# Performance work log

Measured on AMD Instinct MI355X. Metric: run time of the kernel, lower is better.

## Reference

```python
import jax, jax.numpy as jnp
import numpy as np

B, A, I, D = 4, 32, 512, 256


def setup_inputs() -> dict:
    key = jax.random.key(0)
    k0, k1, kw1, kw2, ka1, ka2 = jax.random.split(key, 6)
    return {
        "i0": jax.random.normal(k0, (B, A, I, D), dtype=jnp.float32),
        "i1": jax.random.normal(k1, (B, A, I, D), dtype=jnp.float32),
        "W1": jax.random.normal(kw1, (D, D), dtype=jnp.float32) * 0.02,
        "W2": jax.random.normal(kw2, (D, D), dtype=jnp.float32) * 0.02,
        "attn1": jax.random.normal(ka1, (D, D), dtype=jnp.float32) * 0.02,
        "attn2": jax.random.normal(ka2, (D, D), dtype=jnp.float32) * 0.02,
    }


def reference(i0, i1, W1, W2, attn1, attn2):
    # Bilinear gating scores: sum_j sum_k x1[...,j] * A[j,k] * x0[...,k] -> [b,a,i]
    g0 = jax.nn.sigmoid(jnp.einsum('baij,jk,baik->bai', i1, attn1, i0))
    g1 = jax.nn.sigmoid(jnp.einsum('baij,jk,baik->bai', i0, attn2, i1))
    # Gated residual: x += x * gate
    r0 = i0 + i0 * g0[..., None]
    r1 = i1 + i1 * g1[..., None]
    # Dual projection sum
    return jnp.einsum('baij,jk->baik', r0, W1) + jnp.einsum('baij,jk->baik', r1, W2)
```

## Files before the change

### kernel.cpp

```cpp
#include <hip/hip_runtime.h>

#define D256 256
#define TOTROWS 65536
#define BM 32
#define LDW 264
#define NBLK (TOTROWS / BM)
#define NT 512

typedef unsigned short u16;
typedef unsigned int u32;
typedef __attribute__((ext_vector_type(8))) short bf16x8;
typedef __attribute__((ext_vector_type(16))) float f32x16;

__device__ __forceinline__ float b2f(u16 u) {
  union { u32 i; float f; } v; v.i = ((u32)u) << 16; return v.f;
}
__device__ __forceinline__ u16 f2b(float f) {
  union { float f; u32 i; } v; v.f = f;
  return (u16)((v.i + 0x7fffu + ((v.i >> 16) & 1u)) >> 16);
}
__device__ __forceinline__ u32 f2b2(float lo, float hi) {
  u32 r;
  asm("v_cvt_pk_bf16_f32 %0, %1, %2" : "=v"(r) : "v"(lo), "v"(hi));
  return r;
}

__global__ void build_wfrag(const float* __restrict__ a1,
                            const float* __restrict__ a2,
                            const float* __restrict__ W1,
                            const float* __restrict__ W2,
                            u16* __restrict__ Wf) {
  const int m = blockIdx.y;
  const int idx = blockIdx.x * 256 + threadIdx.x;
  int col, c;
  const float* src;
  if (m < 2) { col = idx >> 5; c = idx & 31; src = m ? a2 : a1; }
  else       { col = idx & 255; c = idx >> 8; src = (m == 3) ? W2 : W1; }
  const int kk0 = c * 8;
  const int p = col >> 5, l31 = col & 31, lhh = c & 1, k = c >> 1;
  const int ln = lhh * 32 + l31;
  u16* dst = Wf + m * 65536 + ((p * 16 + k) * 64 + ln) * 8;
  u16 v[8];
  if (m < 2) {
#pragma unroll
    for (int j = 0; j < 8; j++) v[j] = f2b(src[col * 256 + kk0 + j]);
  } else {
#pragma unroll
    for (int j = 0; j < 8; j++) v[j] = f2b(src[(kk0 + j) * 256 + col]);
  }
  ushort4 lo, hi;
  lo.x = v[0]; lo.y = v[1]; lo.z = v[2]; lo.w = v[3];
  hi.x = v[4]; hi.y = v[5]; hi.z = v[6]; hi.w = v[7];
  ((ushort4*)dst)[0] = lo;
  ((ushort4*)dst)[1] = hi;
}

__device__ __forceinline__ void reduce_accum(float v[16], float* sp,
                                             int l31, int lh) {
#pragma unroll
  for (int r = 0; r < 8; r++) {
    float a = v[r]     + __shfl_xor(v[r],     1, 32);
    float b = v[r + 8] + __shfl_xor(v[r + 8], 1, 32);
    v[r] = (l31 & 1) ? b : a;
  }
#pragma unroll
  for (int r = 0; r < 4; r++) {
    float a = v[r]     + __shfl_xor(v[r],     2, 32);
    float b = v[r + 4] + __shfl_xor(v[r + 4], 2, 32);
    v[r] = (l31 & 2) ? b : a;
  }
#pragma unroll
  for (int r = 0; r < 2; r++) {
    float a = v[r]     + __shfl_xor(v[r],     4, 32);
    float b = v[r + 2] + __shfl_xor(v[r + 2], 4, 32);
    v[r] = (l31 & 4) ? b : a;
  }
  {
    float a = v[0] + __shfl_xor(v[0], 8, 32);
    float b = v[1] + __shfl_xor(v[1], 8, 32);
    v[0] = (l31 & 8) ? b : a;
  }
  v[0] += __shfl_xor(v[0], 16, 32);
  if (l31 < 16) {
    const int i = ((l31 & 1) << 3) | ((l31 & 2) << 1) | ((l31 & 4) >> 1) |
                  ((l31 & 8) >> 3);
    const int row = (i & 3) + 8 * (i >> 2) + 4 * lh;
    atomicAdd(&sp[row], v[0]);
  }
}

__global__ __launch_bounds__(NT, 4)
void fused(const float* __restrict__ X0g, const float* __restrict__ X1g,
           const u16* __restrict__ Wf, float* __restrict__ outg) {
  __shared__ u16 lX0[BM][LDW];
  __shared__ u16 lX1[BM][LDW];
  __shared__ float sp0[BM], sp1[BM];

  const int t = threadIdx.x;
  const int row0 = blockIdx.x * BM;

  if (t < BM) sp0[t] = 0.f;
  else if (t < 2 * BM) sp1[t - BM] = 0.f;

  {
    const float4* g0 = (const float4*)(X0g + (size_t)row0 * D256);
    const float4* g1 = (const float4*)(X1g + (size_t)row0 * D256);
    uint2* s0 = (uint2*)&lX0[0][0];
    uint2* s1 = (uint2*)&lX1[0][0];
#pragma unroll
    for (int i = 0; i < 4; i++) {
      const int e = i * NT + t;
      const int row = e >> 6;
      const int col = e & 63;
      float4 a = g0[e];
      float4 b = g1[e];
      uint2 pa, pb;
      pa.x = f2b2(a.x, a.y); pa.y = f2b2(a.z, a.w);
      pb.x = f2b2(b.x, b.y); pb.y = f2b2(b.z, b.w);
      s0[row * 66 + col] = pa;
      s1[row * 66 + col] = pb;
    }
  }
  __syncthreads();

  const int ln  = t & 63;
  const int wv  = t >> 6;
  const int l31 = ln & 31;
  const int lh  = ln >> 5;
  const int cb  = wv * 32;

  const u16* wA1 = Wf + 0 * 65536 + (wv * 16) * 512 + ln * 8;
  const u16* wA2 = Wf + 1 * 65536 + (wv * 16) * 512 + ln * 8;
  const u16* wW1 = Wf + 2 * 65536 + (wv * 16) * 512 + ln * 8;
  const u16* wW2 = Wf + 3 * 65536 + (wv * 16) * 512 + ln * 8;

  f32x16 G0, G1, P0, P1;
#pragma unroll
  for (int i = 0; i < 16; i++) { G0[i] = 0.f; G1[i] = 0.f;
                                 P0[i] = 0.f; P1[i] = 0.f; }

#pragma unroll 4
  for (int k = 0; k < 16; k++) {
    bf16x8 af0 = *(const bf16x8*)(&lX0[l31][k * 16 + lh * 8]);
    bf16x8 af1 = *(const bf16x8*)(&lX1[l31][k * 16 + lh * 8]);
    bf16x8 wa1 = *(const bf16x8*)(wA1 + k * 512);
    bf16x8 wa2 = *(const bf16x8*)(wA2 + k * 512);
    bf16x8 ww1 = *(const bf16x8*)(wW1 + k * 512);
    bf16x8 ww2 = *(const bf16x8*)(wW2 + k * 512);
    G0 = __builtin_amdgcn_mfma_f32_32x32x16_bf16(af0, wa1, G0, 0, 0, 0);
    P0 = __builtin_amdgcn_mfma_f32_32x32x16_bf16(af0, ww1, P0, 0, 0, 0);
    G1 = __builtin_amdgcn_mfma_f32_32x32x16_bf16(af1, wa2, G1, 0, 0, 0);
    P1 = __builtin_amdgcn_mfma_f32_32x32x16_bf16(af1, ww2, P1, 0, 0, 0);
  }

  {
    float v[16];
#pragma unroll
    for (int r = 0; r < 16; r++) {
      const int row = (r & 3) + 8 * (r >> 2) + 4 * lh;
      v[r] = G0[r] * b2f(lX1[row][cb + l31]);
    }
    reduce_accum(v, sp0, l31, lh);
#pragma unroll
    for (int r = 0; r < 16; r++) {
      const int row = (r & 3) + 8 * (r >> 2) + 4 * lh;
      v[r] = G1[r] * b2f(lX0[row][cb + l31]);
    }
    reduce_accum(v, sp1, l31, lh);
  }
  __syncthreads();

  {
    float* opb = outg + (size_t)row0 * 256 + cb;
#pragma unroll
    for (int q = 0; q < 4; q++) {
#pragma unroll
      for (int j = 0; j < 4; j++) {
        const int r = q * 4 + j;
        const int row = j + 8 * q + 4 * lh;
        const float s0 = 1.f + 1.f / (1.f + __expf(-sp0[row]));
        const float s1 = 1.f + 1.f / (1.f + __expf(-sp1[row]));
        __builtin_nontemporal_store(s0 * P0[r] + s1 * P1[r],
                                    &opb[row * 256 + l31]);
      }
    }
  }
}

extern "C" void kernel_launch(void* const* d_in, const int* in_sizes, int n_in,
                              void* d_out, int out_size, void* d_ws, size_t ws_size,
                              hipStream_t stream) {
  const float* i0 = (const float*)d_in[0];
  const float* i1 = (const float*)d_in[1];
  const float* W1 = (const float*)d_in[2];
  const float* W2 = (const float*)d_in[3];
  const float* a1 = (const float*)d_in[4];
  const float* a2 = (const float*)d_in[5];
  u16* Wf = (u16*)d_ws;

  build_wfrag<<<dim3(32, 4), 256, 0, stream>>>(a1, a2, W1, W2, Wf);
  fused<<<NBLK, NT, 0, stream>>>(i0, i1, Wf, (float*)d_out);
}
```

Before: 218.6 us.

## Tile 64 rows per block with 2x2 register blocking and split gate/projection phases

Doubles the rows per block to 64 and halves the threads to 256, so each wave computes two column tiles for two row tiles. Each weight fragment loaded from global/L2 now feeds two MFMAs, which halves weight traffic per row. The gate GEMMs and projection GEMMs run as separate phases so only 8 accumulator tiles are live at once, and the sigmoid scales are precomputed once per row into shared memory. In exchange, LDS use per block doubles and occupancy drops (launch bounds 2), and the X fragments are read from LDS twice.

```diff
diff --git a/kernel.cpp b/kernel.cpp
--- a/kernel.cpp
+++ b/kernel.cpp
@@ -2,10 +2,10 @@
 
 #define D256 256
 #define TOTROWS 65536
-#define BM 32
+#define BM 64
 #define LDW 264
 #define NBLK (TOTROWS / BM)
-#define NT 512
+#define NT 256
 
 typedef unsigned short u16;
 typedef unsigned int u32;
@@ -89,12 +89,12 @@
   }
 }
 
-__global__ __launch_bounds__(NT, 4)
+__global__ __launch_bounds__(NT, 2)
 void fused(const float* __restrict__ X0g, const float* __restrict__ X1g,
            const u16* __restrict__ Wf, float* __restrict__ outg) {
   __shared__ u16 lX0[BM][LDW];
   __shared__ u16 lX1[BM][LDW];
-  __shared__ float sp0[BM], sp1[BM];
+  __shared__ float sp0[BM], sp1[BM], sc0[BM], sc1[BM];
 
   const int t = threadIdx.x;
   const int row0 = blockIdx.x * BM;
@@ -107,8 +107,8 @@
     const float4* g1 = (const float4*)(X1g + (size_t)row0 * D256);
     uint2* s0 = (uint2*)&lX0[0][0];
     uint2* s1 = (uint2*)&lX1[0][0];
-#pragma unroll
-    for (int i = 0; i < 4; i++) {
+#pragma unroll 4
+    for (int i = 0; i < 16; i++) {
       const int e = i * NT + t;
       const int row = e >> 6;
       const int col = e & 63;
@@ -127,61 +127,114 @@
   const int wv  = t >> 6;
   const int l31 = ln & 31;
   const int lh  = ln >> 5;
-  const int cb  = wv * 32;
-
-  const u16* wA1 = Wf + 0 * 65536 + (wv * 16) * 512 + ln * 8;
-  const u16* wA2 = Wf + 1 * 65536 + (wv * 16) * 512 + ln * 8;
-  const u16* wW1 = Wf + 2 * 65536 + (wv * 16) * 512 + ln * 8;
-  const u16* wW2 = Wf + 3 * 65536 + (wv * 16) * 512 + ln * 8;
-
-  f32x16 G0, G1, P0, P1;
-#pragma unroll
-  for (int i = 0; i < 16; i++) { G0[i] = 0.f; G1[i] = 0.f;
-                                 P0[i] = 0.f; P1[i] = 0.f; }
+  const int cb0 = (2 * wv) * 32;
+  const int cb1 = (2 * wv + 1) * 32;
+
+  const u16* wb[4][2];
+#pragma unroll
+  for (int m = 0; m < 4; m++) {
+#pragma unroll
+    for (int pp = 0; pp < 2; pp++) {
+      wb[m][pp] = Wf + m * 65536 + ((2 * wv + pp) * 16) * 512 + ln * 8;
+    }
+  }
+
+  {
+    f32x16 G[2][2][2];
+#pragma unroll
+    for (int a = 0; a < 2; a++)
+#pragma unroll
+      for (int b = 0; b < 2; b++)
+#pragma unroll
+        for (int c = 0; c < 2; c++)
+#pragma unroll
+          for (int i = 0; i < 16; i++) G[a][b][c][i] = 0.f;
 
 #pragma unroll 4
-  for (int k = 0; k < 16; k++) {
-    bf16x8 af0 = *(const bf16x8*)(&lX0[l31][k * 16 + lh * 8]);
-    bf16x8 af1 = *(const bf16x8*)(&lX1[l31][k * 16 + lh * 8]);
-    bf16x8 wa1 = *(const bf16x8*)(wA1 + k * 512);
-    bf16x8 wa2 = *(const bf16x8*)(wA2 + k * 512);
-    bf16x8 ww1 = *(const bf16x8*)(wW1 + k * 512);
-    bf16x8 ww2 = *(const bf16x8*)(wW2 + k * 512);
-    G0 = __builtin_amdgcn_mfma_f32_32x32x16_bf16(af0, wa1, G0, 0, 0, 0);
-    P0 = __builtin_amdgcn_mfma_f32_32x32x16_bf16(af0, ww1, P0, 0, 0, 0);
-    G1 = __builtin_amdgcn_mfma_f32_32x32x16_bf16(af1, wa2, G1, 0, 0, 0);
-    P1 = __builtin_amdgcn_mfma_f32_32x32x16_bf16(af1, ww2, P1, 0, 0, 0);
-  }
-
-  {
-    float v[16];
-#pragma unroll
-    for (int r = 0; r < 16; r++) {
-      const int row = (r & 3) + 8 * (r >> 2) + 4 * lh;
-      v[r] = G0[r] * b2f(lX1[row][cb + l31]);
-    }
-    reduce_accum(v, sp0, l31, lh);
-#pragma unroll
-    for (int r = 0; r < 16; r++) {
-      const int row = (r & 3) + 8 * (r >> 2) + 4 * lh;
-      v[r] = G1[r] * b2f(lX0[row][cb + l31]);
-    }
-    reduce_accum(v, sp1, l31, lh);
+    for (int k = 0; k < 16; k++) {
+      bf16x8 af0a = *(const bf16x8*)(&lX0[l31][k * 16 + lh * 8]);
+      bf16x8 af0b = *(const bf16x8*)(&lX0[32 + l31][k * 16 + lh * 8]);
+      bf16x8 af1a = *(const bf16x8*)(&lX1[l31][k * 16 + lh * 8]);
+      bf16x8 af1b = *(const bf16x8*)(&lX1[32 + l31][k * 16 + lh * 8]);
+#pragma unroll
+      for (int pp = 0; pp < 2; pp++) {
+        bf16x8 wa1 = *(const bf16x8*)(wb[0][pp] + k * 512);
+        bf16x8 wa2 = *(const bf16x8*)(wb[1][pp] + k * 512);
+        G[pp][0][0] = __builtin_amdgcn_mfma_f32_32x32x16_bf16(af0a, wa1, G[pp][0][0], 0, 0, 0);
+        G[pp][0][1] = __builtin_amdgcn_mfma_f32_32x32x16_bf16(af0b, wa1, G[pp][0][1], 0, 0, 0);
+        G[pp][1][0] = __builtin_amdgcn_mfma_f32_32x32x16_bf16(af1a, wa2, G[pp][1][0], 0, 0, 0);
+        G[pp][1][1] = __builtin_amdgcn_mfma_f32_32x32x16_bf16(af1b, wa2, G[pp][1][1], 0, 0, 0);
+      }
+    }
+
+#pragma unroll
+    for (int tt = 0; tt < 2; tt++) {
+      float v0[16], v1[16];
+#pragma unroll
+      for (int r = 0; r < 16; r++) {
+        const int row = tt * 32 + (r & 3) + 8 * (r >> 2) + 4 * lh;
+        v0[r] = G[0][0][tt][r] * b2f(lX1[row][cb0 + l31]) +
+                G[1][0][tt][r] * b2f(lX1[row][cb1 + l31]);
+        v1[r] = G[0][1][tt][r] * b2f(lX0[row][cb0 + l31]) +
+                G[1][1][tt][r] * b2f(lX0[row][cb1 + l31]);
+      }
+      reduce_accum(v0, sp0 + tt * 32, l31, lh);
+      reduce_accum(v1, sp1 + tt * 32, l31, lh);
+    }
   }
   __syncthreads();
 
-  {
-    float* opb = outg + (size_t)row0 * 256 + cb;
-#pragma unroll
-    for (int q = 0; q < 4; q++) {
-#pragma unroll
-      for (int j = 0; j < 4; j++) {
-        const int r = q * 4 + j;
-        const int row = j + 8 * q + 4 * lh;
-        const float s0 = 1.f + 1.f / (1.f + __expf(-sp0[row]));
-        const float s1 = 1.f + 1.f / (1.f + __expf(-sp1[row]));
-        __builtin_nontemporal_store(s0 * P0[r] + s1 * P1[r],
-                                    &opb[row * 256 + l31]);
+  if (t < BM)          sc0[t] = 1.f + 1.f / (1.f + __expf(-sp0[t]));
+  else if (t < 2 * BM) sc1[t - BM] = 1.f + 1.f / (1.f + __expf(-sp1[t - BM]));
+  __syncthreads();
+
+  {
+    f32x16 P[2][2][2];
+#pragma unroll
+    for (int a = 0; a < 2; a++)
+#pragma unroll
+      for (int b = 0; b < 2; b++)
+#pragma unroll
+        for (int c = 0; c < 2; c++)
+#pragma unroll
+          for (int i = 0; i < 16; i++) P[a][b][c][i] = 0.f;
+
+#pragma unroll 4
+    for (int k = 0; k < 16; k++) {
+      bf16x8 af0a = *(const bf16x8*)(&lX0[l31][k * 16 + lh * 8]);
+      bf16x8 af0b = *(const bf16x8*)(&lX0[32 + l31][k * 16 + lh * 8]);
+      bf16x8 af1a = *(const bf16x8*)(&lX1[l31][k * 16 + lh * 8]);
+      bf16x8 af1b = *(const bf16x8*)(&lX1[32 + l31][k * 16 + lh * 8]);
+#pragma unroll
+      for (int pp = 0; pp < 2; pp++) {
+        bf16x8 ww1 = *(const bf16x8*)(wb[2][pp] + k * 512);
+        bf16x8 ww2 = *(const bf16x8*)(wb[3][pp] + k * 512);
+        P[pp][0][0] = __builtin_amdgcn_mfma_f32_32x32x16_bf16(af0a, ww1, P[pp][0][0], 0, 0, 0);
+        P[pp][0][1] = __builtin_amdgcn_mfma_f32_32x32x16_bf16(af0b, ww1, P[pp][0][1], 0, 0, 0);
+        P[pp][1][0] = __builtin_amdgcn_mfma_f32_32x32x16_bf16(af1a, ww2, P[pp][1][0], 0, 0, 0);
+        P[pp][1][1] = __builtin_amdgcn_mfma_f32_32x32x16_bf16(af1b, ww2, P[pp][1][1], 0, 0, 0);
+      }
+    }
+
+#pragma unroll
+    for (int tt = 0; tt < 2; tt++) {
+#pragma unroll
+      for (int pp = 0; pp < 2; pp++) {
+        float* opb = outg + (size_t)(row0 + tt * 32) * D256 + (pp ? cb1 : cb0);
+#pragma unroll
+        for (int q = 0; q < 4; q++) {
+          float s0a[4], s1a[4];
+          *(float4*)s0a = *(const float4*)&sc0[tt * 32 + 8 * q + 4 * lh];
+          *(float4*)s1a = *(const float4*)&sc1[tt * 32 + 8 * q + 4 * lh];
+#pragma unroll
+          for (int j = 0; j < 4; j++) {
+            const int r = q * 4 + j;
+            const int row = j + 8 * q + 4 * lh;
+            __builtin_nontemporal_store(
+                s0a[j] * P[pp][0][tt][r] + s1a[j] * P[pp][1][tt][r],
+                &opb[row * D256 + l31]);
+          }
+        }
       }
     }
   }
```

New measurement: 220.0 us. Within noise of the previous version (+0.6%).
